# Kernel tuning notes

Measured on AMD Instinct MI355X. Metric: run time of the kernel, lower is better.

The kernel has to match this reference:

```python
import jax, jax.numpy as jnp
import numpy as np

B, SQ, SKV, D = 4, 2048, 2048, 768
H, HD = 12, 16  # num_heads, reduced head_dim (64 / reduce_factor 4)
DR = H * HD     # 192 reduced width


def setup_inputs() -> dict:
    key = jax.random.key(0)
    ks = jax.random.split(key, 6)
    s = 0.02
    return {
        "hidden_states": jax.random.normal(ks[0], (B, SQ, D), jnp.float32),
        "encoder_hidden_states": jax.random.normal(ks[1], (B, SKV, D), jnp.float32),
        "Wq": jax.random.normal(ks[2], (D, DR), jnp.float32) * s,
        "bq": jnp.zeros((DR,), jnp.float32),
        "Wkv": jax.random.normal(ks[3], (D, 2 * DR), jnp.float32) * s,
        "bkv": jnp.zeros((2 * DR,), jnp.float32),
        "Wp": jax.random.normal(ks[4], (DR, D), jnp.float32) * s,
        "bp": jnp.zeros((D,), jnp.float32),
    }


def _split_heads(x):
    # [B, S, DR] -> [B, H, S, HD]
    b, s, _ = x.shape
    return x.reshape(b, s, H, HD).transpose(0, 2, 1, 3)


def reference(hidden_states, encoder_hidden_states, Wq, bq, Wkv, bkv, Wp, bp):
    # Conv1D projections (x @ W + b)
    q = hidden_states @ Wq + bq                       # [B, SQ, 192]
    kv = encoder_hidden_states @ Wkv + bkv            # [B, SKV, 384]
    k, v = kv[..., :DR], kv[..., DR:]
    q = _split_heads(q)                               # [B, H, SQ, HD]
    k = _split_heads(k)                               # [B, H, SKV, HD]
    v = _split_heads(v)                               # [B, H, SKV, HD]
    scale = jnp.asarray(HD, q.dtype) ** 0.5
    scores = jnp.einsum('bhqd,bhkd->bhqk', q, k) / scale
    attn = jax.nn.softmax(scores, axis=-1)            # dropout is identity in eval
    out = jnp.einsum('bhqk,bhkd->bhqd', attn, v)      # [B, H, SQ, HD]
    out = out.transpose(0, 2, 1, 3).reshape(hidden_states.shape[0], -1, DR)
    out = out @ Wp + bp                               # [B, SQ, 768]
    return out
```

## Files before the change

kernel.cpp:

```cpp
#include <hip/hip_runtime.h>
#include <hip/hip_bf16.h>
#include <math.h>

#define NB 4
#define NSQ 2048
#define NSKV 2048
#define ND 768
#define NH 12
#define NHD 16
#define NDR 192
#define M_TOT (NB * NSQ)

typedef __attribute__((ext_vector_type(8)))  short          bf16x8;
typedef __attribute__((ext_vector_type(16))) float          f32x16;
typedef __attribute__((ext_vector_type(8)))  unsigned short u16x8;

__device__ __forceinline__ unsigned short bfbits(float x) {
  __hip_bfloat16 h = __float2bfloat16(x);
  unsigned short u; __builtin_memcpy(&u, &h, 2); return u;
}
__device__ __forceinline__ float bf2f(unsigned short u) {
  unsigned int v = ((unsigned int)u) << 16; float f; __builtin_memcpy(&f, &v, 4); return f;
}
__device__ __forceinline__ unsigned int pk2t(float a, float b) {
  unsigned int ua, ub;
  __builtin_memcpy(&ua, &a, 4); __builtin_memcpy(&ub, &b, 4);
#if __has_builtin(__builtin_amdgcn_perm)
  return __builtin_amdgcn_perm(ub, ua, 0x07060302);
#else
  return (ua >> 16) | (ub & 0xffff0000u);
#endif
}
__device__ __forceinline__ float exp2_raw(float x) {
#if __has_builtin(__builtin_amdgcn_exp2f)
  return __builtin_amdgcn_exp2f(x);
#else
  float r; asm("v_exp_f32 %0, %1" : "=v"(r) : "v"(x)); return r;
#endif
}
__device__ __forceinline__ void g2l16(const void* g, void* l) {
  __builtin_amdgcn_global_load_lds(
      (const __attribute__((address_space(1))) void*)g,
      (__attribute__((address_space(3))) void*)l, 16, 0, 0);
}

#define QSCALE 0.36067376022224085f
#define LDSBUF 16384

__global__ __launch_bounds__(256) void prep(
    const float* __restrict__ Wq, const float* __restrict__ Wkv,
    const float* __restrict__ Wp,
    unsigned short* __restrict__ WSq, unsigned short* __restrict__ WSkv,
    unsigned short* __restrict__ WSp) {
  int bid = blockIdx.x;
  const float* W; unsigned short* out; int Nn, KBLK, bx, by;
  if (bid < 72)        { W = Wq;  out = WSq;  Nn = 192; KBLK = 24; bx = bid % 24;        by = bid / 24; }
  else if (bid < 216)  { int b = bid - 72;  W = Wkv; out = WSkv; Nn = 384; KBLK = 24; bx = b % 24; by = b / 24; }
  else                 { int b = bid - 216; W = Wp;  out = WSp;  Nn = 768; KBLK = 6;  bx = b % 6;  by = b / 6;  }

  __shared__ float tile[32][65];
  int k0 = bx * 32, n0 = by * 64;
  int t = threadIdx.x;
  int kr = t >> 3, c0 = (t & 7) * 8;
  const float* src = W + (size_t)(k0 + kr) * Nn + n0 + c0;
  float4 f0 = *reinterpret_cast<const float4*>(src);
  float4 f1 = *reinterpret_cast<const float4*>(src + 4);
  tile[kr][c0+0] = f0.x; tile[kr][c0+1] = f0.y; tile[kr][c0+2] = f0.z; tile[kr][c0+3] = f0.w;
  tile[kr][c0+4] = f1.x; tile[kr][c0+5] = f1.y; tile[kr][c0+6] = f1.z; tile[kr][c0+7] = f1.w;
  __syncthreads();
  int n = t >> 2, cq0 = (t & 3) * 2;
  int ng = n0 + n, sw = ng & 7;
  unsigned short* dst = out + ((size_t)ng * KBLK + bx) * 64;
  #pragma unroll
  for (int q = 0; q < 2; ++q) {
    int cc = cq0 + q;
    u16x8 v;
    #pragma unroll
    for (int i = 0; i < 8; ++i) {
      float x = tile[(cc & 3) * 8 + i][n];
      unsigned short h = bfbits(x);
      v[i] = (cc < 4) ? h : bfbits(x - bf2f(h));
    }
    *reinterpret_cast<u16x8*>(dst + (cc ^ sw) * 8) = v;
  }
}

__device__ __forceinline__ void core_compute(
    const unsigned short* const (&ard)[4], const unsigned short* const (&wrd)[12],
    int off, f32x16 (&acc)[3]) {
  #pragma unroll
  for (int kk = 0; kk < 2; ++kk) {
    bf16x8 ah = *reinterpret_cast<const bf16x8*>(ard[kk*2+0] + off);
    bf16x8 al = *reinterpret_cast<const bf16x8*>(ard[kk*2+1] + off);
    #pragma unroll
    for (int nr = 0; nr < 3; ++nr) {
      bf16x8 wh = *reinterpret_cast<const bf16x8*>(wrd[(nr*2+kk)*2+0] + off);
      bf16x8 wl = *reinterpret_cast<const bf16x8*>(wrd[(nr*2+kk)*2+1] + off);
      acc[nr] = __builtin_amdgcn_mfma_f32_32x32x16_bf16(ah, wh, acc[nr], 0, 0, 0);
      acc[nr] = __builtin_amdgcn_mfma_f32_32x32x16_bf16(ah, wl, acc[nr], 0, 0, 0);
      acc[nr] = __builtin_amdgcn_mfma_f32_32x32x16_bf16(al, wh, acc[nr], 0, 0, 0);
    }
  }
}

__device__ __forceinline__ void gemm_core(
    const unsigned short* __restrict__ As,
    const unsigned short* __restrict__ Ws,
    const float* __restrict__ bias,
    int KBLK, unsigned short* lds, f32x16 (&acc)[3]) {
  const int tid = threadIdx.x;
  const int wv = tid >> 6, lane = tid & 63;
  const int l31 = lane & 31, hi8 = lane >> 5;
  const int wm = wv >> 1, wn = wv & 1;

  unsigned short* Ab = lds;
  unsigned short* Wb = lds + 64 * 64;

  const int r8 = lane >> 3, c8 = lane & 7;
  const size_t rowu = (size_t)KBLK * 64;

  const unsigned short* srcA0 = As + (size_t)((0*4 + wv)*8 + r8) * rowu + c8*8;
  const unsigned short* srcA1 = As + (size_t)((1*4 + wv)*8 + r8) * rowu + c8*8;
  const unsigned short* srcW[6];
  #pragma unroll
  for (int j = 0; j < 6; ++j)
    srcW[j] = Ws + (size_t)((j*4 + wv)*8 + r8) * rowu + c8*8;

  unsigned short* dA0 = Ab + ((0*4 + wv)*64 + lane) * 8;
  unsigned short* dA1 = Ab + ((1*4 + wv)*64 + lane) * 8;
  unsigned short* dW[6];
  #pragma unroll
  for (int j = 0; j < 6; ++j)
    dW[j] = Wb + ((j*4 + wv)*64 + lane) * 8;

  const int ra = wm*32 + l31;
  const unsigned short* ard[4];
  #pragma unroll
  for (int kk = 0; kk < 2; ++kk) {
    ard[kk*2+0] = Ab + ra*64 + (((kk*2 + hi8)     ^ (ra & 7)) * 8);
    ard[kk*2+1] = Ab + ra*64 + (((4 + kk*2 + hi8) ^ (ra & 7)) * 8);
  }
  const unsigned short* wrd[12];
  #pragma unroll
  for (int nr = 0; nr < 3; ++nr) {
    int rw = wn*96 + nr*32 + l31;
    #pragma unroll
    for (int kk = 0; kk < 2; ++kk) {
      wrd[(nr*2+kk)*2+0] = Wb + rw*64 + (((kk*2 + hi8)     ^ (rw & 7)) * 8);
      wrd[(nr*2+kk)*2+1] = Wb + rw*64 + (((4 + kk*2 + hi8) ^ (rw & 7)) * 8);
    }
  }

  #pragma unroll
  for (int nr = 0; nr < 3; ++nr) {
    float bv = bias[wn*96 + nr*32 + l31];
    #pragma unroll
    for (int r = 0; r < 16; ++r) acc[nr][r] = bv;
  }

  g2l16(srcA0, dA0); srcA0 += 64;
  g2l16(srcA1, dA1); srcA1 += 64;
  #pragma unroll
  for (int j = 0; j < 6; ++j) { g2l16(srcW[j], dW[j]); srcW[j] += 64; }
  __syncthreads();

  for (int kb = 0; kb < KBLK; kb += 2) {
    if (kb + 1 < KBLK) {
      g2l16(srcA0, dA0 + LDSBUF); srcA0 += 64;
      g2l16(srcA1, dA1 + LDSBUF); srcA1 += 64;
      #pragma unroll
      for (int j = 0; j < 6; ++j) { g2l16(srcW[j], dW[j] + LDSBUF); srcW[j] += 64; }
    }
    core_compute(ard, wrd, 0, acc);
    __syncthreads();
    if (kb + 2 < KBLK) {
      g2l16(srcA0, dA0); srcA0 += 64;
      g2l16(srcA1, dA1); srcA1 += 64;
      #pragma unroll
      for (int j = 0; j < 6; ++j) { g2l16(srcW[j], dW[j]); srcW[j] += 64; }
    }
    core_compute(ard, wrd, LDSBUF, acc);
    __syncthreads();
  }
}

#define QHALF 10240
__global__ __launch_bounds__(384) void gemm_qkv(
    const float* __restrict__ A1, const float* __restrict__ A2,
    const unsigned short* __restrict__ WSq, const unsigned short* __restrict__ WSkv,
    const float* __restrict__ bq, const float* __restrict__ bkv,
    unsigned short* __restrict__ Qbf, unsigned short* __restrict__ Kbf,
    unsigned short* __restrict__ VTbf) {
  __shared__ unsigned short lds[2 * QHALF];
  const int bid = blockIdx.x;
  const float* Afp; const unsigned short* Ws; const float* bias;
  int m0, mode, ntile;
  if (bid < 256) {
    mode = 0; ntile = (bid >> 7) * 96;
    Afp = A1; Ws = WSq + (size_t)ntile * (24*64); bias = bq + ntile;
    m0 = (bid & 127) * 64;
  } else {
    int b2 = bid - 256;
    int sub = b2 >> 7;
    m0 = (b2 & 127) * 64;
    Afp = A2;
    if (sub < 2) { mode = 1; ntile = sub * 96;
                   Ws = WSkv + (size_t)ntile * (24*64); bias = bkv + ntile; }
    else         { mode = 2; ntile = (sub - 2) * 96;
                   Ws = WSkv + (size_t)(192 + ntile) * (24*64); bias = bkv + 192 + ntile; }
  }
  Afp += (size_t)m0 * ND;

  const int tid = threadIdx.x;
  const int wv = tid >> 6, lane = tid & 63;
  const int l31 = lane & 31, hi8 = lane >> 5;
  const int wm = wv & 1, wn = wv >> 1;

  unsigned short* Ab = lds;
  unsigned short* Wb = lds + 64*64;

  const int ar = tid >> 2, cq = tid & 3;
  const bool doA = (tid < 256);
  const float* srcA = Afp + (size_t)(doA ? ar : 0) * ND + cq*8;
  unsigned short* dAh = Ab + (doA ? ar : 0)*64 + ((cq       ^ (ar & 7)) * 8);
  unsigned short* dAl = Ab + (doA ? ar : 0)*64 + (((cq + 4) ^ (ar & 7)) * 8);

  const int wch0 = tid, wch1 = tid + 384;
  const unsigned short* srcW0 = Ws + (size_t)(wch0 >> 3) * (24*64) + (wch0 & 7) * 8;
  const unsigned short* srcW1 = Ws + (size_t)(wch1 >> 3) * (24*64) + (wch1 & 7) * 8;
  unsigned short* dW0 = Wb + wch0 * 8;
  unsigned short* dW1 = Wb + wch1 * 8;

  const int ra = wm*32 + l31;
  const int rw = wn*32 + l31;
  const unsigned short* ard[4];
  const unsigned short* wrd[4];
  #pragma unroll
  for (int kk = 0; kk < 2; ++kk) {
    ard[kk*2+0] = Ab + ra*64 + (((kk*2 + hi8)     ^ (ra & 7)) * 8);
    ard[kk*2+1] = Ab + ra*64 + (((4 + kk*2 + hi8) ^ (ra & 7)) * 8);
    wrd[kk*2+0] = Wb + rw*64 + (((kk*2 + hi8)     ^ (rw & 7)) * 8);
    wrd[kk*2+1] = Wb + rw*64 + (((4 + kk*2 + hi8) ^ (rw & 7)) * 8);
  }

  f32x16 acc;
  {
    float bv = bias[wn*32 + l31];
    #pragma unroll
    for (int r = 0; r < 16; ++r) acc[r] = bv;
  }

  {
    g2l16(srcW0, dW0); srcW0 += 64;
    g2l16(srcW1, dW1); srcW1 += 64;
    if (doA) {
      float4 f0 = *reinterpret_cast<const float4*>(srcA);
      float4 f1 = *reinterpret_cast<const float4*>(srcA + 4);
      float x[8] = {f0.x, f0.y, f0.z, f0.w, f1.x, f1.y, f1.z, f1.w};
      u16x8 hv, lv;
      #pragma unroll
      for (int i = 0; i < 8; ++i) {
        unsigned short h = bfbits(x[i]);
        hv[i] = h; lv[i] = bfbits(x[i] - bf2f(h));
      }
      *reinterpret_cast<u16x8*>(dAh) = hv;
      *reinterpret_cast<u16x8*>(dAl) = lv;
    }
    srcA += 32;
  }
  __syncthreads();

  #define QKV_COMPUTE(off)                                                     \
    {                                                                          \
      _Pragma("unroll")                                                        \
      for (int kk = 0; kk < 2; ++kk) {                                         \
        bf16x8 ah = *reinterpret_cast<const bf16x8*>(ard[kk*2+0] + (off));     \
        bf16x8 al = *reinterpret_cast<const bf16x8*>(ard[kk*2+1] + (off));     \
        bf16x8 wh = *reinterpret_cast<const bf16x8*>(wrd[kk*2+0] + (off));     \
        bf16x8 wl = *reinterpret_cast<const bf16x8*>(wrd[kk*2+1] + (off));     \
        acc = __builtin_amdgcn_mfma_f32_32x32x16_bf16(ah, wh, acc, 0, 0, 0);   \
        acc = __builtin_amdgcn_mfma_f32_32x32x16_bf16(ah, wl, acc, 0, 0, 0);   \
        acc = __builtin_amdgcn_mfma_f32_32x32x16_bf16(al, wh, acc, 0, 0, 0);   \
      }                                                                        \
    }

  for (int kb = 0; kb < 24; kb += 2) {
    float4 f0, f1;
    g2l16(srcW0, dW0 + QHALF); srcW0 += 64;
    g2l16(srcW1, dW1 + QHALF); srcW1 += 64;
    if (doA) {
      f0 = *reinterpret_cast<const float4*>(srcA);
      f1 = *reinterpret_cast<const float4*>(srcA + 4);
    }
    srcA += 32;
    QKV_COMPUTE(0)
    if (doA) {
      float x[8] = {f0.x, f0.y, f0.z, f0.w, f1.x, f1.y, f1.z, f1.w};
      u16x8 hv, lv;
      #pragma unroll
      for (int i = 0; i < 8; ++i) {
        unsigned short h = bfbits(x[i]);
        hv[i] = h; lv[i] = bfbits(x[i] - bf2f(h));
      }
      *reinterpret_cast<u16x8*>(dAh + QHALF) = hv;
      *reinterpret_cast<u16x8*>(dAl + QHALF) = lv;
    }
    __syncthreads();
    bool has2 = (kb + 2 < 24);
    if (has2) {
      g2l16(srcW0, dW0); srcW0 += 64;
      g2l16(srcW1, dW1); srcW1 += 64;
      if (doA) {
        f0 = *reinterpret_cast<const float4*>(srcA);
        f1 = *reinterpret_cast<const float4*>(srcA + 4);
      }
      srcA += 32;
    }
    QKV_COMPUTE(QHALF)
    if (has2 && doA) {
      float x[8] = {f0.x, f0.y, f0.z, f0.w, f1.x, f1.y, f1.z, f1.w};
      u16x8 hv, lv;
      #pragma unroll
      for (int i = 0; i < 8; ++i) {
        unsigned short h = bfbits(x[i]);
        hv[i] = h; lv[i] = bfbits(x[i] - bf2f(h));
      }
      *reinterpret_cast<u16x8*>(dAh) = hv;
      *reinterpret_cast<u16x8*>(dAl) = lv;
    }
    __syncthreads();
  }
  #undef QKV_COMPUTE

  if (mode == 2) {
    unsigned short (*tile)[65] = reinterpret_cast<unsigned short(*)[65]>(lds);
    #pragma unroll
    for (int r = 0; r < 16; ++r) {
      int key_l = wm*32 + (r & 3) + 8*(r >> 2) + 4*hi8;
      tile[wn*32 + l31][key_l] = bfbits(acc[r]);
    }
    __syncthreads();
    int b = m0 >> 11, key0 = m0 & 2047;
    #pragma unroll
    for (int j = 0; j < 2; ++j) {
      int flat = j * 384 + tid;
      int row = flat >> 3;
      int ck = flat & 7;
      int vcol = ntile + row;
      int h = vcol >> 4, d = vcol & 15;
      u16x8 v;
      #pragma unroll
      for (int jj = 0; jj < 8; ++jj) v[jj] = tile[row][ck*8 + jj];
      *reinterpret_cast<u16x8*>(
          &VTbf[(((size_t)(b*NH + h)*256 + (key0 >> 3) + ck)*16 + d)*8]) = v;
    }
    return;
  }

  unsigned short* outp = (mode == 0) ? Qbf : Kbf;
  const float scale = (mode == 0) ? QSCALE : 1.0f;
  {
    int col = ntile + wn*32 + l31;
    int h = col >> 4, d = col & 15;
    #pragma unroll
    for (int r = 0; r < 16; ++r) {
      int mg = m0 + wm*32 + (r & 3) + 8*(r >> 2) + 4*hi8;
      int b = mg >> 11, q = mg & 2047;
      outp[(((size_t)b*NH + h)*NSQ + q)*16 + d] = bfbits(acc[r] * scale);
    }
  }
}

__device__ __forceinline__ void attn_tile32(
    bf16x8 qf, bf16x8 kf, bf16x8 vf0, bf16x8 vf1,
    int hi8, const f32x16& zeroc, f32x16& acc) {
  f32x16 s = __builtin_amdgcn_mfma_f32_32x32x16_bf16(kf, qf, zeroc, 0, 0, 0);

  float p[16];
  #pragma unroll
  for (int r = 0; r < 16; ++r) p[r] = exp2_raw(s[r]);

  unsigned int w[8];
  #pragma unroll
  for (int t8 = 0; t8 < 8; ++t8) w[t8] = pk2t(p[2*t8], p[2*t8+1]);

  unsigned int t0 = hi8 ? w[0] : w[2], t1 = hi8 ? w[1] : w[3];
  unsigned int t2 = hi8 ? w[4] : w[6], t3 = hi8 ? w[5] : w[7];
  unsigned int r0 = (unsigned int)__shfl_xor((int)t0, 32);
  unsigned int r1 = (unsigned int)__shfl_xor((int)t1, 32);
  unsigned int r2 = (unsigned int)__shfl_xor((int)t2, 32);
  unsigned int r3 = (unsigned int)__shfl_xor((int)t3, 32);

  union { bf16x8 v; unsigned int u[4]; } pa0, pa1;
  pa0.u[0] = hi8 ? r0 : w[0];  pa0.u[1] = hi8 ? r1 : w[1];
  pa0.u[2] = hi8 ? w[2] : r0;  pa0.u[3] = hi8 ? w[3] : r1;
  pa1.u[0] = hi8 ? r2 : w[4];  pa1.u[1] = hi8 ? r3 : w[5];
  pa1.u[2] = hi8 ? w[6] : r2;  pa1.u[3] = hi8 ? w[7] : r3;

  __builtin_amdgcn_s_setprio(1);
  acc = __builtin_amdgcn_mfma_f32_32x32x16_bf16(vf0, pa0.v, acc, 0, 0, 0);
  acc = __builtin_amdgcn_mfma_f32_32x32x16_bf16(vf1, pa1.v, acc, 0, 0, 0);
  __builtin_amdgcn_s_setprio(0);
}

__global__ __launch_bounds__(256, 4) void attn_bf16(
    const unsigned short* __restrict__ Qbf, const unsigned short* __restrict__ Kbf,
    const unsigned short* __restrict__ VT, unsigned short* __restrict__ AOS) {
  __shared__ float comb[4][64][9];
  const int tid = threadIdx.x;
  const int wave = tid >> 6, lane = tid & 63;
  const int l31 = lane & 31, hi8 = lane >> 5;
  const int bid = blockIdx.x;
  const int bh = bid % 48;
  const int qt = bid / 48;
  const int q = qt * 32 + l31;

  bf16x8 qf = *reinterpret_cast<const bf16x8*>(&Qbf[((size_t)bh*NSQ + q)*16 + hi8*8]);
  const unsigned short* kbase = Kbf + (size_t)bh * NSKV * 16;

  const short fillv = (l31 == 16) ? (short)0x3F80 : (short)0;
  bf16x8 vfill;
  #pragma unroll
  for (int j = 0; j < 8; ++j) vfill[j] = fillv;

  f32x16 acc;
  #pragma unroll
  for (int r = 0; r < 16; ++r) acc[r] = 0.f;
  const f32x16 zeroc = acc;

  const int kstart = wave * (NSKV / 4);
  const unsigned short* kp = &kbase[(size_t)(kstart + l31)*16 + hi8*8];
  const unsigned short* vwave = VT + ((((size_t)bh*256 + (kstart >> 3) + hi8)*16 + l31) * 8);

  bf16x8 k0, v00, v10;
  bf16x8 k1, v01, v11;

  k0  = *reinterpret_cast<const bf16x8*>(kp);
  v00 = vfill; v10 = vfill;
  if (l31 < 16) {
    v00 = *reinterpret_cast<const bf16x8*>(vwave);
    v10 = *reinterpret_cast<const bf16x8*>(vwave + 256);
  }

  for (int kt = 0; kt < 512; kt += 64) {
    {
      k1 = *reinterpret_cast<const bf16x8*>(kp + (size_t)(kt + 32) * 16);
      v01 = vfill; v11 = vfill;
      if (l31 < 16) {
        const unsigned short* vq = vwave + (size_t)(kt + 32) * 16;
        v01 = *reinterpret_cast<const bf16x8*>(vq);
        v11 = *reinterpret_cast<const bf16x8*>(vq + 256);
      }
    }
    attn_tile32(qf, k0, v00, v10, hi8, zeroc, acc);
    if (kt + 64 < 512) {
      k0 = *reinterpret_cast<const bf16x8*>(kp + (size_t)(kt + 64) * 16);
      v00 = vfill; v10 = vfill;
      if (l31 < 16) {
        const unsigned short* vq = vwave + (size_t)(kt + 64) * 16;
        v00 = *reinterpret_cast<const bf16x8*>(vq);
        v10 = *reinterpret_cast<const bf16x8*>(vq + 256);
      }
    }
    attn_tile32(qf, k1, v01, v11, hi8, zeroc, acc);
  }

  {
    float* cb = &comb[wave][lane][0];
    #pragma unroll
    for (int r = 0; r < 9; ++r) cb[r] = acc[r];
  }
  __syncthreads();

  if (wave == 0) {
    float A[9];
    #pragma unroll
    for (int r = 0; r < 9; ++r)
      A[r] = ((comb[0][lane][r] + comb[1][lane][r]) +
              (comb[2][lane][r] + comb[3][lane][r]));
    float L = A[8] + __shfl_xor(A[8], 32);
    float inv = 1.f / L;

    unsigned short oh[8], ol[8];
    #pragma unroll
    for (int r = 0; r < 8; ++r) {
      float o = A[r] * inv;
      oh[r] = bfbits(o);
      ol[r] = bfbits(o - bf2f(oh[r]));
    }
    int b = bh / NH, h = bh % NH;
    int mrow = b * NSQ + q;
    unsigned short* rowp = AOS + (size_t)mrow * (6 * 64);
    int sw = mrow & 7;
    int kblk = h >> 1;
    int cA = (h & 1) * 2;
    unsigned short* p0;
    p0 = rowp + ((kblk*8 + ((cA + 0) ^ sw)) * 8) + 4*hi8;
    reinterpret_cast<unsigned int*>(p0)[0] = (unsigned)oh[0] | ((unsigned)oh[1] << 16);
    reinterpret_cast<unsigned int*>(p0)[1] = (unsigned)oh[2] | ((unsigned)oh[3] << 16);
    p0 = rowp + ((kblk*8 + ((cA + 1) ^ sw)) * 8) + 4*hi8;
    reinterpret_cast<unsigned int*>(p0)[0] = (unsigned)oh[4] | ((unsigned)oh[5] << 16);
    reinterpret_cast<unsigned int*>(p0)[1] = (unsigned)oh[6] | ((unsigned)oh[7] << 16);
    p0 = rowp + ((kblk*8 + ((cA + 4) ^ sw)) * 8) + 4*hi8;
    reinterpret_cast<unsigned int*>(p0)[0] = (unsigned)ol[0] | ((unsigned)ol[1] << 16);
    reinterpret_cast<unsigned int*>(p0)[1] = (unsigned)ol[2] | ((unsigned)ol[3] << 16);
    p0 = rowp + ((kblk*8 + ((cA + 5) ^ sw)) * 8) + 4*hi8;
    reinterpret_cast<unsigned int*>(p0)[0] = (unsigned)ol[4] | ((unsigned)ol[5] << 16);
    reinterpret_cast<unsigned int*>(p0)[1] = (unsigned)ol[6] | ((unsigned)ol[7] << 16);
  }
}

__global__ __launch_bounds__(256) void gemm_out_k(
    const unsigned short* __restrict__ AOS, const unsigned short* __restrict__ WSp,
    const float* __restrict__ bp, float* __restrict__ out) {
  __shared__ unsigned short lds[2 * LDSBUF];
  const int bid = blockIdx.x;
  const int KBLK = NDR / 32;
  int m0 = (bid & 127) * 64;
  int n0 = (bid >> 7) * 192;
  const unsigned short* As = AOS + (size_t)m0 * KBLK * 64;
  const unsigned short* Ws = WSp + (size_t)n0 * KBLK * 64;
  f32x16 acc[3];
  gemm_core(As, Ws, bp + n0, KBLK, lds, acc);

  const int tid = threadIdx.x;
  const int wv = tid >> 6, lane = tid & 63;
  const int l31 = lane & 31, hi8 = lane >> 5;
  const int wm = wv >> 1, wn = wv & 1;
  #pragma unroll
  for (int nr = 0; nr < 3; ++nr) {
    int n = n0 + wn*96 + nr*32 + l31;
    #pragma unroll
    for (int r = 0; r < 16; ++r) {
      int mg = m0 + wm*32 + (r & 3) + 8*(r >> 2) + 4*hi8;
      out[(size_t)mg * ND + n] = acc[nr][r];
    }
  }
}

extern "C" void kernel_launch(void* const* d_in, const int* in_sizes, int n_in,
                              void* d_out, int out_size, void* d_ws, size_t ws_size,
                              hipStream_t stream) {
  const float* hs  = (const float*)d_in[0];
  const float* ehs = (const float*)d_in[1];
  const float* Wq  = (const float*)d_in[2];
  const float* bq  = (const float*)d_in[3];
  const float* Wkv = (const float*)d_in[4];
  const float* bkv = (const float*)d_in[5];
  const float* Wp  = (const float*)d_in[6];
  const float* bp  = (const float*)d_in[7];
  float* out = (float*)d_out;

  char* w = (char*)d_ws;
  unsigned short* AOS = (unsigned short*)w;
  char* w2 = w + (size_t)M_TOT * 6 * 64 * 2;
  unsigned short* WSq  = (unsigned short*)w2;
  unsigned short* WSkv = (unsigned short*)(w2 + 589824);
  unsigned short* WSp  = (unsigned short*)(w2 + 589824 + 1179648);
  char* w3 = w2 + 589824 + 1179648 + 589824;
  unsigned short* Qbf  = (unsigned short*)w3;
  unsigned short* Kbf  = Qbf + (size_t)M_TOT * NDR;
  unsigned short* VTbf = Kbf + (size_t)M_TOT * NDR;

  prep<<<dim3(72 + 144 + 72), dim3(256), 0, stream>>>(
      Wq, Wkv, Wp, WSq, WSkv, WSp);
  gemm_qkv<<<dim3(768), dim3(384), 0, stream>>>(hs, ehs, WSq, WSkv, bq, bkv, Qbf, Kbf, VTbf);
  attn_bf16<<<dim3(NB * NH * 64), dim3(256), 0, stream>>>(Qbf, Kbf, VTbf, AOS);
  gemm_out_k<<<dim3(512), dim3(256), 0, stream>>>(AOS, WSp, bp, out);
}
```

Baseline: 84.19 us.

## Process two 32-query tiles per attention block to reuse K/V fragments

Each attention workgroup now handles 64 queries (two 32-row Q fragments) instead of 32. Every loaded K/V fragment therefore feeds two score MFMAs and two PV accumulations, halving K/V global loads per query, and the grid shrinks to half as many blocks. The cost is more registers per wave (launch bounds lowered from 4 to 3 waves-per-SIMD), twice the LDS combine buffer, two waves doing the final reduction, and fewer blocks (1536) to fill the GPU.

```diff
diff --git a/kernel.cpp b/kernel.cpp
--- a/kernel.cpp
+++ b/kernel.cpp
@@ -371,51 +371,68 @@
   }
 }
 
-__device__ __forceinline__ void attn_tile32(
-    bf16x8 qf, bf16x8 kf, bf16x8 vf0, bf16x8 vf1,
-    int hi8, const f32x16& zeroc, f32x16& acc) {
-  f32x16 s = __builtin_amdgcn_mfma_f32_32x32x16_bf16(kf, qf, zeroc, 0, 0, 0);
-
-  float p[16];
-  #pragma unroll
-  for (int r = 0; r < 16; ++r) p[r] = exp2_raw(s[r]);
-
-  unsigned int w[8];
-  #pragma unroll
-  for (int t8 = 0; t8 < 8; ++t8) w[t8] = pk2t(p[2*t8], p[2*t8+1]);
-
-  unsigned int t0 = hi8 ? w[0] : w[2], t1 = hi8 ? w[1] : w[3];
-  unsigned int t2 = hi8 ? w[4] : w[6], t3 = hi8 ? w[5] : w[7];
-  unsigned int r0 = (unsigned int)__shfl_xor((int)t0, 32);
-  unsigned int r1 = (unsigned int)__shfl_xor((int)t1, 32);
-  unsigned int r2 = (unsigned int)__shfl_xor((int)t2, 32);
-  unsigned int r3 = (unsigned int)__shfl_xor((int)t3, 32);
-
-  union { bf16x8 v; unsigned int u[4]; } pa0, pa1;
-  pa0.u[0] = hi8 ? r0 : w[0];  pa0.u[1] = hi8 ? r1 : w[1];
-  pa0.u[2] = hi8 ? w[2] : r0;  pa0.u[3] = hi8 ? w[3] : r1;
-  pa1.u[0] = hi8 ? r2 : w[4];  pa1.u[1] = hi8 ? r3 : w[5];
-  pa1.u[2] = hi8 ? w[6] : r2;  pa1.u[3] = hi8 ? w[7] : r3;
+__device__ __forceinline__ void attn_tile32x2(
+    bf16x8 qfA, bf16x8 qfB, bf16x8 kf, bf16x8 vf0, bf16x8 vf1,
+    int hi8, const f32x16& zeroc, f32x16& accA, f32x16& accB) {
+  f32x16 sA = __builtin_amdgcn_mfma_f32_32x32x16_bf16(kf, qfA, zeroc, 0, 0, 0);
+  f32x16 sB = __builtin_amdgcn_mfma_f32_32x32x16_bf16(kf, qfB, zeroc, 0, 0, 0);
+
+  float pA[16], pB[16];
+  #pragma unroll
+  for (int r = 0; r < 16; ++r) { pA[r] = exp2_raw(sA[r]); pB[r] = exp2_raw(sB[r]); }
+
+  unsigned int wA[8], wB[8];
+  #pragma unroll
+  for (int t8 = 0; t8 < 8; ++t8) {
+    wA[t8] = pk2t(pA[2*t8], pA[2*t8+1]);
+    wB[t8] = pk2t(pB[2*t8], pB[2*t8+1]);
+  }
+
+  unsigned int tA0 = hi8 ? wA[0] : wA[2], tA1 = hi8 ? wA[1] : wA[3];
+  unsigned int tA2 = hi8 ? wA[4] : wA[6], tA3 = hi8 ? wA[5] : wA[7];
+  unsigned int tB0 = hi8 ? wB[0] : wB[2], tB1 = hi8 ? wB[1] : wB[3];
+  unsigned int tB2 = hi8 ? wB[4] : wB[6], tB3 = hi8 ? wB[5] : wB[7];
+  unsigned int rA0 = (unsigned int)__shfl_xor((int)tA0, 32);
+  unsigned int rA1 = (unsigned int)__shfl_xor((int)tA1, 32);
+  unsigned int rA2 = (unsigned int)__shfl_xor((int)tA2, 32);
+  unsigned int rA3 = (unsigned int)__shfl_xor((int)tA3, 32);
+  unsigned int rB0 = (unsigned int)__shfl_xor((int)tB0, 32);
+  unsigned int rB1 = (unsigned int)__shfl_xor((int)tB1, 32);
+  unsigned int rB2 = (unsigned int)__shfl_xor((int)tB2, 32);
+  unsigned int rB3 = (unsigned int)__shfl_xor((int)tB3, 32);
+
+  union { bf16x8 v; unsigned int u[4]; } pa0A, pa1A, pa0B, pa1B;
+  pa0A.u[0] = hi8 ? rA0 : wA[0];  pa0A.u[1] = hi8 ? rA1 : wA[1];
+  pa0A.u[2] = hi8 ? wA[2] : rA0;  pa0A.u[3] = hi8 ? wA[3] : rA1;
+  pa1A.u[0] = hi8 ? rA2 : wA[4];  pa1A.u[1] = hi8 ? rA3 : wA[5];
+  pa1A.u[2] = hi8 ? wA[6] : rA2;  pa1A.u[3] = hi8 ? wA[7] : rA3;
+  pa0B.u[0] = hi8 ? rB0 : wB[0];  pa0B.u[1] = hi8 ? rB1 : wB[1];
+  pa0B.u[2] = hi8 ? wB[2] : rB0;  pa0B.u[3] = hi8 ? wB[3] : rB1;
+  pa1B.u[0] = hi8 ? rB2 : wB[4];  pa1B.u[1] = hi8 ? rB3 : wB[5];
+  pa1B.u[2] = hi8 ? wB[6] : rB2;  pa1B.u[3] = hi8 ? wB[7] : rB3;
 
   __builtin_amdgcn_s_setprio(1);
-  acc = __builtin_amdgcn_mfma_f32_32x32x16_bf16(vf0, pa0.v, acc, 0, 0, 0);
-  acc = __builtin_amdgcn_mfma_f32_32x32x16_bf16(vf1, pa1.v, acc, 0, 0, 0);
+  accA = __builtin_amdgcn_mfma_f32_32x32x16_bf16(vf0, pa0A.v, accA, 0, 0, 0);
+  accB = __builtin_amdgcn_mfma_f32_32x32x16_bf16(vf0, pa0B.v, accB, 0, 0, 0);
+  accA = __builtin_amdgcn_mfma_f32_32x32x16_bf16(vf1, pa1A.v, accA, 0, 0, 0);
+  accB = __builtin_amdgcn_mfma_f32_32x32x16_bf16(vf1, pa1B.v, accB, 0, 0, 0);
   __builtin_amdgcn_s_setprio(0);
 }
 
-__global__ __launch_bounds__(256, 4) void attn_bf16(
+__global__ __launch_bounds__(256, 3) void attn_bf16(
     const unsigned short* __restrict__ Qbf, const unsigned short* __restrict__ Kbf,
     const unsigned short* __restrict__ VT, unsigned short* __restrict__ AOS) {
-  __shared__ float comb[4][64][9];
+  __shared__ float comb[2][4][64][9];
   const int tid = threadIdx.x;
   const int wave = tid >> 6, lane = tid & 63;
   const int l31 = lane & 31, hi8 = lane >> 5;
   const int bid = blockIdx.x;
   const int bh = bid % 48;
   const int qt = bid / 48;
-  const int q = qt * 32 + l31;
-
-  bf16x8 qf = *reinterpret_cast<const bf16x8*>(&Qbf[((size_t)bh*NSQ + q)*16 + hi8*8]);
+
+  const unsigned short* qp = &Qbf[((size_t)bh*NSQ + qt*64 + l31)*16 + hi8*8];
+  bf16x8 qfA = *reinterpret_cast<const bf16x8*>(qp);
+  bf16x8 qfB = *reinterpret_cast<const bf16x8*>(qp + 32*16);
   const unsigned short* kbase = Kbf + (size_t)bh * NSKV * 16;
 
   const short fillv = (l31 == 16) ? (short)0x3F80 : (short)0;
@@ -423,10 +440,10 @@
   #pragma unroll
   for (int j = 0; j < 8; ++j) vfill[j] = fillv;
 
-  f32x16 acc;
-  #pragma unroll
-  for (int r = 0; r < 16; ++r) acc[r] = 0.f;
-  const f32x16 zeroc = acc;
+  f32x16 accA, accB;
+  #pragma unroll
+  for (int r = 0; r < 16; ++r) { accA[r] = 0.f; accB[r] = 0.f; }
+  const f32x16 zeroc = accA;
 
   const int kstart = wave * (NSKV / 4);
   const unsigned short* kp = &kbase[(size_t)(kstart + l31)*16 + hi8*8];
@@ -452,7 +469,7 @@
         v11 = *reinterpret_cast<const bf16x8*>(vq + 256);
       }
     }
-    attn_tile32(qf, k0, v00, v10, hi8, zeroc, acc);
+    attn_tile32x2(qfA, qfB, k0, v00, v10, hi8, zeroc, accA, accB);
     if (kt + 64 < 512) {
       k0 = *reinterpret_cast<const bf16x8*>(kp + (size_t)(kt + 64) * 16);
       v00 = vfill; v10 = vfill;
@@ -462,22 +479,24 @@
         v10 = *reinterpret_cast<const bf16x8*>(vq + 256);
       }
     }
-    attn_tile32(qf, k1, v01, v11, hi8, zeroc, acc);
+    attn_tile32x2(qfA, qfB, k1, v01, v11, hi8, zeroc, accA, accB);
   }
 
   {
-    float* cb = &comb[wave][lane][0];
-    #pragma unroll
-    for (int r = 0; r < 9; ++r) cb[r] = acc[r];
+    float* cbA = &comb[0][wave][lane][0];
+    float* cbB = &comb[1][wave][lane][0];
+    #pragma unroll
+    for (int r = 0; r < 9; ++r) { cbA[r] = accA[r]; cbB[r] = accB[r]; }
   }
   __syncthreads();
 
-  if (wave == 0) {
+  if (wave < 2) {
+    const int g = wave;
     float A[9];
     #pragma unroll
     for (int r = 0; r < 9; ++r)
-      A[r] = ((comb[0][lane][r] + comb[1][lane][r]) +
-              (comb[2][lane][r] + comb[3][lane][r]));
+      A[r] = ((comb[g][0][lane][r] + comb[g][1][lane][r]) +
+              (comb[g][2][lane][r] + comb[g][3][lane][r]));
     float L = A[8] + __shfl_xor(A[8], 32);
     float inv = 1.f / L;
 
@@ -489,6 +508,7 @@
       ol[r] = bfbits(o - bf2f(oh[r]));
     }
     int b = bh / NH, h = bh % NH;
+    int q = qt*64 + g*32 + l31;
     int mrow = b * NSQ + q;
     unsigned short* rowp = AOS + (size_t)mrow * (6 * 64);
     int sw = mrow & 7;
@@ -565,6 +585,6 @@
   prep<<<dim3(72 + 144 + 72), dim3(256), 0, stream>>>(
       Wq, Wkv, Wp, WSq, WSkv, WSp);
   gemm_qkv<<<dim3(768), dim3(384), 0, stream>>>(hs, ehs, WSq, WSkv, bq, bkv, Qbf, Kbf, VTbf);
-  attn_bf16<<<dim3(NB * NH * 64), dim3(256), 0, stream>>>(Qbf, Kbf, VTbf, AOS);
+  attn_bf16<<<dim3(NB * NH * 32), dim3(256), 0, stream>>>(Qbf, Kbf, VTbf, AOS);
   gemm_out_k<<<dim3(512), dim3(256), 0, stream>>>(AOS, WSp, bp, out);
 }
```

Result: no change. 83.16 us (-1.2%).
